# Kernel tuning notes

Hardware: AMD Instinct MI355X
Metric: run time of the kernel (lower is better)

Reference implementation:

```python
import jax, jax.numpy as jnp
import numpy as np

DIM = 128
N = 1024


def setup_inputs() -> dict:
    key = jax.random.key(0)
    ks = jax.random.split(key, 11)
    s = 1.0 / np.sqrt(DIM)
    # Linear params stored as [in, out] (y = x @ W + b), matching torch math.
    return {
        "x": jax.random.normal(ks[0], (N, DIM), jnp.float32),
        "W_Q": jax.random.uniform(ks[1], (DIM, DIM), jnp.float32, -s, s),
        "b_Q": jax.random.uniform(ks[2], (DIM,), jnp.float32, -s, s),
        "W_K": jax.random.uniform(ks[3], (DIM, DIM), jnp.float32, -s, s),
        "b_K": jax.random.uniform(ks[4], (DIM,), jnp.float32, -s, s),
        "W_V": jax.random.uniform(ks[5], (DIM, DIM), jnp.float32, -s, s),
        "b_V": jax.random.uniform(ks[6], (DIM,), jnp.float32, -s, s),
        "W_Ev": jax.random.uniform(ks[7], (DIM, DIM), jnp.float32, -s, s),
        "b_Ev": jax.random.uniform(ks[8], (DIM,), jnp.float32, -s, s),
        "W_A": jax.random.uniform(ks[9], (DIM, 1), jnp.float32, -s, s),
        "b_A": jax.random.uniform(ks[10], (1,), jnp.float32, -s, s),
    }


def reference(x, W_Q, b_Q, W_K, b_K, W_V, b_V, W_Ev, b_Ev, W_A, b_A):
    Q = x @ W_Q + b_Q                               # [n, d]
    K = x @ W_K + b_K                               # [n, d]
    V = x @ W_V + b_V                               # [n, d]
    edge_feat = jax.nn.relu(Q[:, None, :] + K[None, :, :])   # [n, n, d]
    e_ij = jnp.squeeze(edge_feat @ W_A, -1) + b_A[0]          # [n, n]
    alpha = jax.nn.softmax(e_ij, axis=1)                      # softmax over j
    EV = edge_feat @ W_Ev + b_Ev                              # [n, n, d]
    # out_i = sum_j alpha_ij * (V_j + EV_ij)
    out = jnp.einsum('ij,ijd->id', alpha, V[None, :, :] + EV)
    return out
```

## Files before the change

### kernel.cpp

```cpp
#include <hip/hip_runtime.h>

#define N 1024
#define DIM 128
#define TI 4
#define JCH 256
#define NCH 4
#define SC 16
#define NSC 16

template <int CTRL>
__device__ __forceinline__ float dpp_add(float x) {
  int y = __builtin_amdgcn_update_dpp(0, __float_as_int(x), CTRL, 0xF, 0xF, true);
  return x + __int_as_float(y);
}
__device__ __forceinline__ float red32(float x) {
  x = dpp_add<0x111>(x);
  x = dpp_add<0x112>(x);
  x = dpp_add<0x114>(x);
  x = dpp_add<0x118>(x);
  x = dpp_add<0x142>(x);
  return x;
}

__device__ __forceinline__ float bperm(int baddr, float x) {
  return __int_as_float(__builtin_amdgcn_ds_bpermute(baddr, __float_as_int(x)));
}

__device__ __forceinline__ float epart_keep(const float4 q, const float4 k,
                                            const float4 w, float4* relu) {
  const float rx = fmaxf(q.x + k.x, 0.f);
  const float ry = fmaxf(q.y + k.y, 0.f);
  const float rz = fmaxf(q.z + k.z, 0.f);
  const float rw = fmaxf(q.w + k.w, 0.f);
  relu->x = rx; relu->y = ry; relu->z = rz; relu->w = rw;
  float a = rx * w.x;
  a = fmaf(ry, w.y, a);
  a = fmaf(rz, w.z, a);
  a = fmaf(rw, w.w, a);
  return a;
}

__device__ __forceinline__ void accum_rs(float p, const float4 relu,
                                         const float4 v, float4* R, float4* S) {
  R->x = fmaf(p, relu.x, R->x);
  R->y = fmaf(p, relu.y, R->y);
  R->z = fmaf(p, relu.z, R->z);
  R->w = fmaf(p, relu.w, R->w);
  S->x = fmaf(p, v.x, S->x);
  S->y = fmaf(p, v.y, S->y);
  S->z = fmaf(p, v.z, S->z);
  S->w = fmaf(p, v.w, S->w);
}

__global__ __launch_bounds__(512) void qkv_kernel3(
    const float* __restrict__ x,
    const float* __restrict__ WQ, const float* __restrict__ bQ,
    const float* __restrict__ WK, const float* __restrict__ bK,
    const float* __restrict__ WV, const float* __restrict__ bV,
    float* __restrict__ Q, float* __restrict__ K, float* __restrict__ V) {
  const int i0 = blockIdx.x * 4;
  const int t = threadIdx.x;
  const int dq = t & 31;
  const int qr = t >> 5;

  __shared__ __align__(16) float xs[4][DIM];
  __shared__ __align__(16) float pacc[16][3][4][DIM];

  if (t < 128) {
    const int row = t >> 5, c4 = t & 31;
    ((float4*)&xs[row][0])[c4] = ((const float4*)(x + (i0 + row) * DIM))[c4];
  }
  __syncthreads();

  const float4* WQ4 = (const float4*)WQ;
  const float4* WK4 = (const float4*)WK;
  const float4* WV4 = (const float4*)WV;
  float4 aQ[4], aK[4], aV[4];
#pragma unroll
  for (int r = 0; r < 4; ++r) {
    aQ[r] = make_float4(0.f, 0.f, 0.f, 0.f);
    aK[r] = make_float4(0.f, 0.f, 0.f, 0.f);
    aV[r] = make_float4(0.f, 0.f, 0.f, 0.f);
  }
  const int c0 = qr * 8;
#pragma unroll 2
  for (int cc = 0; cc < 8; ++cc) {
    const int c = c0 + cc;
    const float4 wq = WQ4[c * 32 + dq];
    const float4 wk = WK4[c * 32 + dq];
    const float4 wv = WV4[c * 32 + dq];
#pragma unroll
    for (int r = 0; r < 4; ++r) {
      const float xv = xs[r][c];
      aQ[r].x = fmaf(xv, wq.x, aQ[r].x); aQ[r].y = fmaf(xv, wq.y, aQ[r].y);
      aQ[r].z = fmaf(xv, wq.z, aQ[r].z); aQ[r].w = fmaf(xv, wq.w, aQ[r].w);
      aK[r].x = fmaf(xv, wk.x, aK[r].x); aK[r].y = fmaf(xv, wk.y, aK[r].y);
      aK[r].z = fmaf(xv, wk.z, aK[r].z); aK[r].w = fmaf(xv, wk.w, aK[r].w);
      aV[r].x = fmaf(xv, wv.x, aV[r].x); aV[r].y = fmaf(xv, wv.y, aV[r].y);
      aV[r].z = fmaf(xv, wv.z, aV[r].z); aV[r].w = fmaf(xv, wv.w, aV[r].w);
    }
  }
#pragma unroll
  for (int r = 0; r < 4; ++r) {
    ((float4*)&pacc[qr][0][r][0])[dq] = aQ[r];
    ((float4*)&pacc[qr][1][r][0])[dq] = aK[r];
    ((float4*)&pacc[qr][2][r][0])[dq] = aV[r];
  }
  __syncthreads();
  {
    const int row = (t >> 7) & 3, d = t & 127;
#pragma unroll
    for (int m = 0; m < 3; ++m) {
      float s = 0.f;
#pragma unroll
      for (int c = 0; c < 16; ++c) s += pacc[c][m][row][d];
      float* dst = (m == 0) ? Q : (m == 1) ? K : V;
      const float* bias = (m == 0) ? bQ : (m == 1) ? bK : bV;
      dst[(i0 + row) * DIM + d] = s + bias[d];
    }
  }
}

__global__ __launch_bounds__(256, 4) void attn_fused6(
    const float* __restrict__ Q, const float* __restrict__ K,
    const float* __restrict__ V, const float* __restrict__ WA,
    float* __restrict__ Rw, float* __restrict__ Sw, float* __restrict__ Lw) {
  const int bi = blockIdx.x >> 2;
  const int jc = blockIdx.x & 3;
  const int i0 = bi * TI;
  const int j0 = jc * JCH;
  const int t = threadIdx.x;
  const int dq = t & 31;
  const int f = t >> 5;
  const int baddr = (t & 32) ? (63 << 2) : (31 << 2);

  __shared__ __align__(16) float red_s[2][8 * TI * DIM];
  __shared__ __align__(16) float4 lred4[8];

  float4 wa4 = ((const float4*)WA)[dq];
  const float LOG2E = 1.44269504088896340736f;
  wa4.x *= LOG2E; wa4.y *= LOG2E; wa4.z *= LOG2E; wa4.w *= LOG2E;

  float4 q4[TI];
#pragma unroll
  for (int r = 0; r < TI; ++r)
    q4[r] = ((const float4*)(Q + (i0 + r) * DIM))[dq];

  float4 Racc[TI], Sacc[TI];
#pragma unroll
  for (int r = 0; r < TI; ++r) {
    Racc[r] = make_float4(0.f, 0.f, 0.f, 0.f);
    Sacc[r] = make_float4(0.f, 0.f, 0.f, 0.f);
  }
  float4 lacc = make_float4(0.f, 0.f, 0.f, 0.f);

  const float4* K4 = (const float4*)K;
  const float4* V4 = (const float4*)V;
  float4 kc0 = K4[(j0 + f) * 32 + dq];
  float4 kc1 = K4[(j0 + 8 + f) * 32 + dq];
  float4 vc0 = V4[(j0 + f) * 32 + dq];
  float4 vc1 = V4[(j0 + 8 + f) * 32 + dq];

  for (int sc = 0; sc < NSC; ++sc) {
    const int jb = j0 + ((sc + 1 < NSC) ? sc + 1 : sc) * SC;

    float4 reluA0, reluA1, reluA2, reluA3;
    float4 peA;
    peA.x = epart_keep(q4[0], kc0, wa4, &reluA0);
    peA.y = epart_keep(q4[1], kc0, wa4, &reluA1);
    peA.z = epart_keep(q4[2], kc0, wa4, &reluA2);
    peA.w = epart_keep(q4[3], kc0, wa4, &reluA3);
    kc0 = K4[(jb + f) * 32 + dq];

    peA.x = red32(peA.x); peA.y = red32(peA.y);
    peA.z = red32(peA.z); peA.w = red32(peA.w);
    float4 pA;
    pA.x = __builtin_amdgcn_exp2f(bperm(baddr, peA.x));
    pA.y = __builtin_amdgcn_exp2f(bperm(baddr, peA.y));
    pA.z = __builtin_amdgcn_exp2f(bperm(baddr, peA.z));
    pA.w = __builtin_amdgcn_exp2f(bperm(baddr, peA.w));

    accum_rs(pA.x, reluA0, vc0, &Racc[0], &Sacc[0]);
    accum_rs(pA.y, reluA1, vc0, &Racc[1], &Sacc[1]);
    accum_rs(pA.z, reluA2, vc0, &Racc[2], &Sacc[2]);
    accum_rs(pA.w, reluA3, vc0, &Racc[3], &Sacc[3]);
    vc0 = V4[(jb + f) * 32 + dq];
    lacc.x += pA.x; lacc.y += pA.y; lacc.z += pA.z; lacc.w += pA.w;

    float4 reluB0, reluB1, reluB2, reluB3;
    float4 peB;
    peB.x = epart_keep(q4[0], kc1, wa4, &reluB0);
    peB.y = epart_keep(q4[1], kc1, wa4, &reluB1);
    peB.z = epart_keep(q4[2], kc1, wa4, &reluB2);
    peB.w = epart_keep(q4[3], kc1, wa4, &reluB3);
    kc1 = K4[(jb + 8 + f) * 32 + dq];

    peB.x = red32(peB.x); peB.y = red32(peB.y);
    peB.z = red32(peB.z); peB.w = red32(peB.w);
    float4 pB;
    pB.x = __builtin_amdgcn_exp2f(bperm(baddr, peB.x));
    pB.y = __builtin_amdgcn_exp2f(bperm(baddr, peB.y));
    pB.z = __builtin_amdgcn_exp2f(bperm(baddr, peB.z));
    pB.w = __builtin_amdgcn_exp2f(bperm(baddr, peB.w));

    accum_rs(pB.x, reluB0, vc1, &Racc[0], &Sacc[0]);
    accum_rs(pB.y, reluB1, vc1, &Racc[1], &Sacc[1]);
    accum_rs(pB.z, reluB2, vc1, &Racc[2], &Sacc[2]);
    accum_rs(pB.w, reluB3, vc1, &Racc[3], &Sacc[3]);
    vc1 = V4[(jb + 8 + f) * 32 + dq];
    lacc.x += pB.x; lacc.y += pB.y; lacc.z += pB.z; lacc.w += pB.w;
  }

  float4* F4r = (float4*)&red_s[0][0];
  float4* F4s = (float4*)&red_s[1][0];
#pragma unroll
  for (int r = 0; r < TI; ++r) {
    F4r[(f * 4 + r) * 32 + dq] = Racc[r];
    F4s[(f * 4 + r) * 32 + dq] = Sacc[r];
  }
  if (dq == 0) lred4[f] = lacc;
  __syncthreads();
#pragma unroll
  for (int p = 0; p < 4; ++p) {
    const int o = t + 256 * p;
    const int m = o >> 9;
    const int r = (o >> 7) & 3;
    const int d = o & 127;
    float acc = 0.f;
#pragma unroll
    for (int c = 0; c < 8; ++c) acc += red_s[m][(c * 4 + r) * 128 + d];
    float* dst = m ? Sw : Rw;
    dst[(jc * N + i0 + r) * DIM + d] = acc;
  }
  if (t < TI) {
    float l = 0.f;
#pragma unroll
    for (int c = 0; c < 8; ++c) l += ((const float*)&lred4[c])[t];
    Lw[jc * N + i0 + t] = l;
  }
}

__global__ __launch_bounds__(256) void attn_combine5(
    const float* __restrict__ WEv, const float* __restrict__ bEv,
    const float* __restrict__ Rw, const float* __restrict__ Sw,
    const float* __restrict__ Lw, float* __restrict__ out) {
  const int i0 = blockIdx.x * 2;
  const int t = threadIdx.x;

  __shared__ __align__(16) float Rst[2][DIM];
  __shared__ __align__(16) float Sst[2][DIM];
  __shared__ __align__(16) float4 Eacc4[8][2][DIM / 4];
  __shared__ float linv_s[2];

  if (t < 8) {
    const int row = t >> 2, c = t & 3;
    float l = Lw[c * N + i0 + row];
    l += __shfl_xor(l, 1, 4);
    l += __shfl_xor(l, 2, 4);
    if (c == 0) linv_s[row] = 1.0f / l;
  }

#pragma unroll
  for (int p = 0; p < 2; ++p) {
    const int o = t + 256 * p;
    const int d = o & 127;
    const int set = o >> 7;
    const int row = set & 1;
    const int mat = set >> 1;
    const float* src = mat ? Sw : Rw;
    float acc = 0.f;
#pragma unroll
    for (int c = 0; c < NCH; ++c) acc += src[(c * N + i0 + row) * DIM + d];
    if (mat) Sst[row][d] = acc; else Rst[row][d] = acc;
  }
  __syncthreads();

  {
    const int dq = t & 31;
    const int qr = t >> 5;
    const float4* WEv4 = (const float4*)WEv;
    float4 a0 = make_float4(0.f, 0.f, 0.f, 0.f);
    float4 a1 = make_float4(0.f, 0.f, 0.f, 0.f);
    const int dp0 = 16 * qr;
#pragma unroll 8
    for (int dp = dp0; dp < dp0 + 16; ++dp) {
      const float4 w4 = WEv4[dp * 32 + dq];
      const float r0 = Rst[0][dp];
      const float r1 = Rst[1][dp];
      a0.x = fmaf(r0, w4.x, a0.x); a0.y = fmaf(r0, w4.y, a0.y);
      a0.z = fmaf(r0, w4.z, a0.z); a0.w = fmaf(r0, w4.w, a0.w);
      a1.x = fmaf(r1, w4.x, a1.x); a1.y = fmaf(r1, w4.y, a1.y);
      a1.z = fmaf(r1, w4.z, a1.z); a1.w = fmaf(r1, w4.w, a1.w);
    }
    Eacc4[qr][0][dq] = a0;
    Eacc4[qr][1][dq] = a1;
  }
  __syncthreads();

  {
    const int row = t >> 7, d = t & 127;
    const int dq = d >> 2, e = d & 3;
    float acc = Sst[row][d];
#pragma unroll
    for (int qr = 0; qr < 8; ++qr)
      acc += ((const float*)&Eacc4[qr][row][dq])[e];
    out[(i0 + row) * DIM + d] = fmaf(acc, linv_s[row], bEv[d]);
  }
}

__global__ __launch_bounds__(256) void attn_fallback(
    const float* __restrict__ Q, const float* __restrict__ K,
    const float* __restrict__ V, const float* __restrict__ WA,
    const float* __restrict__ WEv, const float* __restrict__ bEv,
    float* __restrict__ out) {
  const int i = blockIdx.x;
  const int t = threadIdx.x;

  __shared__ __align__(16) float qs[DIM];
  __shared__ __align__(16) float was[DIM];
  __shared__ __align__(16) float p[N];
  __shared__ float red[256];
  __shared__ __align__(16) float Rs[8][DIM];
  __shared__ __align__(16) float Ss[8][DIM];

  if (t < DIM) {
    qs[t] = Q[i * DIM + t];
    was[t] = WA[t];
  }
  __syncthreads();

  float evals[4];
  float mloc = -3.4e38f;
  for (int jj = 0; jj < 4; ++jj) {
    const int j = t + jj * 256;
    const float4* krow = (const float4*)(K + j * DIM);
    const float4* q4p = (const float4*)qs;
    const float4* w4p = (const float4*)was;
    float acc = 0.f;
    for (int d4 = 0; d4 < DIM / 4; ++d4) {
      const float4 k4 = krow[d4];
      const float4 q4 = q4p[d4];
      const float4 w4 = w4p[d4];
      acc = fmaf(fmaxf(q4.x + k4.x, 0.f), w4.x, acc);
      acc = fmaf(fmaxf(q4.y + k4.y, 0.f), w4.y, acc);
      acc = fmaf(fmaxf(q4.z + k4.z, 0.f), w4.z, acc);
      acc = fmaf(fmaxf(q4.w + k4.w, 0.f), w4.w, acc);
    }
    evals[jj] = acc;
    mloc = fmaxf(mloc, acc);
  }
  red[t] = mloc;
  __syncthreads();
  for (int s = 128; s > 0; s >>= 1) {
    if (t < s) red[t] = fmaxf(red[t], red[t + s]);
    __syncthreads();
  }
  const float m = red[0];
  __syncthreads();
  float lsum = 0.f;
  for (int jj = 0; jj < 4; ++jj) {
    const float pe = __expf(evals[jj] - m);
    p[t + jj * 256] = pe;
    lsum += pe;
  }
  red[t] = lsum;
  __syncthreads();
  for (int s = 128; s > 0; s >>= 1) {
    if (t < s) red[t] += red[t + s];
    __syncthreads();
  }
  const float linv = 1.0f / red[0];
  __syncthreads();

  const int tx = t & 31;
  const int ty = t >> 5;
  const float4 q4 = ((const float4*)qs)[tx];
  float4 R4 = make_float4(0.f, 0.f, 0.f, 0.f);
  float4 S4 = make_float4(0.f, 0.f, 0.f, 0.f);
  for (int j = ty; j < N; j += 8) {
    const float pj = p[j];
    const float4 k4 = ((const float4*)(K + j * DIM))[tx];
    const float4 v4 = ((const float4*)(V + j * DIM))[tx];
    R4.x = fmaf(pj, fmaxf(q4.x + k4.x, 0.f), R4.x);
    R4.y = fmaf(pj, fmaxf(q4.y + k4.y, 0.f), R4.y);
    R4.z = fmaf(pj, fmaxf(q4.z + k4.z, 0.f), R4.z);
    R4.w = fmaf(pj, fmaxf(q4.w + k4.w, 0.f), R4.w);
    S4.x = fmaf(pj, v4.x, S4.x);
    S4.y = fmaf(pj, v4.y, S4.y);
    S4.z = fmaf(pj, v4.z, S4.z);
    S4.w = fmaf(pj, v4.w, S4.w);
  }
  ((float4*)&Rs[ty][0])[tx] = R4;
  ((float4*)&Ss[ty][0])[tx] = S4;
  __syncthreads();

  if (t < DIM) {
    float R = 0.f, S = 0.f;
    for (int g = 0; g < 8; ++g) {
      R += Rs[g][t];
      S += Ss[g][t];
    }
    Rs[0][t] = R;
    Ss[0][t] = S;
  }
  __syncthreads();

  if (t < DIM) {
    float o = Ss[0][t];
    for (int dp = 0; dp < DIM; ++dp) {
      o = fmaf(Rs[0][dp], WEv[dp * DIM + t], o);
    }
    out[i * DIM + t] = fmaf(o, linv, bEv[t]);
  }
}

extern "C" void kernel_launch(void* const* d_in, const int* in_sizes, int n_in,
                              void* d_out, int out_size, void* d_ws, size_t ws_size,
                              hipStream_t stream) {
  const float* x    = (const float*)d_in[0];
  const float* W_Q  = (const float*)d_in[1];
  const float* b_Q  = (const float*)d_in[2];
  const float* W_K  = (const float*)d_in[3];
  const float* b_K  = (const float*)d_in[4];
  const float* W_V  = (const float*)d_in[5];
  const float* b_V  = (const float*)d_in[6];
  const float* W_Ev = (const float*)d_in[7];
  const float* b_Ev = (const float*)d_in[8];
  const float* W_A  = (const float*)d_in[9];

  float* Q = (float*)d_ws;
  float* K = Q + N * DIM;
  float* V = K + N * DIM;
  float* out = (float*)d_out;

  const size_t need_floats = (size_t)3 * N * DIM + (size_t)2 * NCH * N * DIM +
                             (size_t)NCH * N;

  qkv_kernel3<<<N / 4, 512, 0, stream>>>(x, W_Q, b_Q, W_K, b_K, W_V, b_V, Q, K, V);

  if (ws_size >= need_floats * sizeof(float)) {
    float* Rw = V + N * DIM;
    float* Sw = Rw + NCH * N * DIM;
    float* Lw = Sw + NCH * N * DIM;
    attn_fused6<<<(N / TI) * NCH, 256, 0, stream>>>(Q, K, V, W_A, Rw, Sw, Lw);
    attn_combine5<<<N / 2, 256, 0, stream>>>(W_Ev, b_Ev, Rw, Sw, Lw, out);
  } else {
    attn_fallback<<<N, 256, 0, stream>>>(Q, K, V, W_A, W_Ev, b_Ev, out);
  }
}
```

Before: 111.0 us.

## Fuse attention split-j and combine kernels into one 1024-thread block per row tile

Replaces the two-kernel scheme (4 j-chunk blocks per 4-row tile writing partial R/S/L to workspace, then a combine kernel) with a single kernel. Each 1024-thread block covers all 1024 j for 4 rows and reduces partials across 32 wavefront groups in shared memory. It then applies W_Ev and the normalization in place. This removes the workspace round trip and one launch, but it cuts the grid from 1024 to 256 blocks and uses much larger shared memory (about 128KB of reduction buffers), which may lower occupancy and parallelism.

```diff
diff --git a/kernel.cpp b/kernel.cpp
--- a/kernel.cpp
+++ b/kernel.cpp
@@ -3,9 +3,7 @@
 #define N 1024
 #define DIM 128
 #define TI 4
-#define JCH 256
-#define NCH 4
-#define SC 16
+#define NG 32
 #define NSC 16
 
 template <int CTRL>
@@ -121,21 +119,22 @@
   }
 }
 
-__global__ __launch_bounds__(256, 4) void attn_fused6(
+__global__ __launch_bounds__(1024) void attn_mono(
     const float* __restrict__ Q, const float* __restrict__ K,
     const float* __restrict__ V, const float* __restrict__ WA,
-    float* __restrict__ Rw, float* __restrict__ Sw, float* __restrict__ Lw) {
-  const int bi = blockIdx.x >> 2;
-  const int jc = blockIdx.x & 3;
-  const int i0 = bi * TI;
-  const int j0 = jc * JCH;
+    const float* __restrict__ WEv, const float* __restrict__ bEv,
+    float* __restrict__ out) {
+  const int i0 = blockIdx.x * TI;
   const int t = threadIdx.x;
   const int dq = t & 31;
   const int f = t >> 5;
   const int baddr = (t & 32) ? (63 << 2) : (31 << 2);
 
-  __shared__ __align__(16) float red_s[2][8 * TI * DIM];
-  __shared__ __align__(16) float4 lred4[8];
+  __shared__ __align__(16) float red_s[2][NG * TI * DIM];
+  __shared__ __align__(16) float4 lred4[NG];
+  __shared__ __align__(16) float Rst[TI][DIM];
+  __shared__ __align__(16) float Sst[TI][DIM];
+  __shared__ float linv_s[TI];
 
   float4 wa4 = ((const float4*)WA)[dq];
   const float LOG2E = 1.44269504088896340736f;
@@ -156,13 +155,13 @@
 
   const float4* K4 = (const float4*)K;
   const float4* V4 = (const float4*)V;
-  float4 kc0 = K4[(j0 + f) * 32 + dq];
-  float4 kc1 = K4[(j0 + 8 + f) * 32 + dq];
-  float4 vc0 = V4[(j0 + f) * 32 + dq];
-  float4 vc1 = V4[(j0 + 8 + f) * 32 + dq];
+  float4 kc0 = K4[(f) * 32 + dq];
+  float4 kc1 = K4[(NG + f) * 32 + dq];
+  float4 vc0 = V4[(f) * 32 + dq];
+  float4 vc1 = V4[(NG + f) * 32 + dq];
 
   for (int sc = 0; sc < NSC; ++sc) {
-    const int jb = j0 + ((sc + 1 < NSC) ? sc + 1 : sc) * SC;
+    const int jb = ((sc + 1 < NSC) ? sc + 1 : sc) * (2 * NG);
 
     float4 reluA0, reluA1, reluA2, reluA3;
     float4 peA;
@@ -193,7 +192,7 @@
     peB.y = epart_keep(q4[1], kc1, wa4, &reluB1);
     peB.z = epart_keep(q4[2], kc1, wa4, &reluB2);
     peB.w = epart_keep(q4[3], kc1, wa4, &reluB3);
-    kc1 = K4[(jb + 8 + f) * 32 + dq];
+    kc1 = K4[(jb + NG + f) * 32 + dq];
 
     peB.x = red32(peB.x); peB.y = red32(peB.y);
     peB.z = red32(peB.z); peB.w = red32(peB.w);
@@ -207,7 +206,7 @@
     accum_rs(pB.y, reluB1, vc1, &Racc[1], &Sacc[1]);
     accum_rs(pB.z, reluB2, vc1, &Racc[2], &Sacc[2]);
     accum_rs(pB.w, reluB3, vc1, &Racc[3], &Sacc[3]);
-    vc1 = V4[(jb + 8 + f) * 32 + dq];
+    vc1 = V4[(jb + NG + f) * 32 + dq];
     lacc.x += pB.x; lacc.y += pB.y; lacc.z += pB.z; lacc.w += pB.w;
   }
 
@@ -220,91 +219,66 @@
   }
   if (dq == 0) lred4[f] = lacc;
   __syncthreads();
-#pragma unroll
-  for (int p = 0; p < 4; ++p) {
-    const int o = t + 256 * p;
-    const int m = o >> 9;
-    const int r = (o >> 7) & 3;
-    const int d = o & 127;
+
+  {
+    const int m = t >> 9;
+    const int r = (t >> 7) & 3;
+    const int d = t & 127;
     float acc = 0.f;
 #pragma unroll
-    for (int c = 0; c < 8; ++c) acc += red_s[m][(c * 4 + r) * 128 + d];
-    float* dst = m ? Sw : Rw;
-    dst[(jc * N + i0 + r) * DIM + d] = acc;
+    for (int c = 0; c < NG; ++c) acc += red_s[m][(c * 4 + r) * 128 + d];
+    if (m) Sst[r][d] = acc; else Rst[r][d] = acc;
   }
   if (t < TI) {
+    const float* lf = (const float*)lred4;
     float l = 0.f;
 #pragma unroll
-    for (int c = 0; c < 8; ++c) l += ((const float*)&lred4[c])[t];
-    Lw[jc * N + i0 + t] = l;
-  }
-}
-
-__global__ __launch_bounds__(256) void attn_combine5(
-    const float* __restrict__ WEv, const float* __restrict__ bEv,
-    const float* __restrict__ Rw, const float* __restrict__ Sw,
-    const float* __restrict__ Lw, float* __restrict__ out) {
-  const int i0 = blockIdx.x * 2;
-  const int t = threadIdx.x;
-
-  __shared__ __align__(16) float Rst[2][DIM];
-  __shared__ __align__(16) float Sst[2][DIM];
-  __shared__ __align__(16) float4 Eacc4[8][2][DIM / 4];
-  __shared__ float linv_s[2];
-
-  if (t < 8) {
-    const int row = t >> 2, c = t & 3;
-    float l = Lw[c * N + i0 + row];
-    l += __shfl_xor(l, 1, 4);
-    l += __shfl_xor(l, 2, 4);
-    if (c == 0) linv_s[row] = 1.0f / l;
-  }
-
-#pragma unroll
-  for (int p = 0; p < 2; ++p) {
-    const int o = t + 256 * p;
-    const int d = o & 127;
-    const int set = o >> 7;
-    const int row = set & 1;
-    const int mat = set >> 1;
-    const float* src = mat ? Sw : Rw;
-    float acc = 0.f;
-#pragma unroll
-    for (int c = 0; c < NCH; ++c) acc += src[(c * N + i0 + row) * DIM + d];
-    if (mat) Sst[row][d] = acc; else Rst[row][d] = acc;
+    for (int c = 0; c < NG; ++c) l += lf[c * 4 + t];
+    linv_s[t] = 1.0f / l;
   }
   __syncthreads();
 
   {
-    const int dq = t & 31;
-    const int qr = t >> 5;
+    const int qr = f;
     const float4* WEv4 = (const float4*)WEv;
     float4 a0 = make_float4(0.f, 0.f, 0.f, 0.f);
     float4 a1 = make_float4(0.f, 0.f, 0.f, 0.f);
-    const int dp0 = 16 * qr;
-#pragma unroll 8
-    for (int dp = dp0; dp < dp0 + 16; ++dp) {
+    float4 a2 = make_float4(0.f, 0.f, 0.f, 0.f);
+    float4 a3 = make_float4(0.f, 0.f, 0.f, 0.f);
+    const int dp0 = 4 * qr;
+#pragma unroll
+    for (int k = 0; k < 4; ++k) {
+      const int dp = dp0 + k;
       const float4 w4 = WEv4[dp * 32 + dq];
       const float r0 = Rst[0][dp];
       const float r1 = Rst[1][dp];
+      const float r2 = Rst[2][dp];
+      const float r3 = Rst[3][dp];
       a0.x = fmaf(r0, w4.x, a0.x); a0.y = fmaf(r0, w4.y, a0.y);
       a0.z = fmaf(r0, w4.z, a0.z); a0.w = fmaf(r0, w4.w, a0.w);
       a1.x = fmaf(r1, w4.x, a1.x); a1.y = fmaf(r1, w4.y, a1.y);
       a1.z = fmaf(r1, w4.z, a1.z); a1.w = fmaf(r1, w4.w, a1.w);
-    }
-    Eacc4[qr][0][dq] = a0;
-    Eacc4[qr][1][dq] = a1;
-  }
-  __syncthreads();
-
-  {
-    const int row = t >> 7, d = t & 127;
-    const int dq = d >> 2, e = d & 3;
-    float acc = Sst[row][d];
-#pragma unroll
-    for (int qr = 0; qr < 8; ++qr)
-      acc += ((const float*)&Eacc4[qr][row][dq])[e];
-    out[(i0 + row) * DIM + d] = fmaf(acc, linv_s[row], bEv[d]);
+      a2.x = fmaf(r2, w4.x, a2.x); a2.y = fmaf(r2, w4.y, a2.y);
+      a2.z = fmaf(r2, w4.z, a2.z); a2.w = fmaf(r2, w4.w, a2.w);
+      a3.x = fmaf(r3, w4.x, a3.x); a3.y = fmaf(r3, w4.y, a3.y);
+      a3.z = fmaf(r3, w4.z, a3.z); a3.w = fmaf(r3, w4.w, a3.w);
+    }
+    float4* Eq = (float4*)&red_s[0][0];
+    Eq[(qr * 4 + 0) * 32 + dq] = a0;
+    Eq[(qr * 4 + 1) * 32 + dq] = a1;
+    Eq[(qr * 4 + 2) * 32 + dq] = a2;
+    Eq[(qr * 4 + 3) * 32 + dq] = a3;
+  }
+  __syncthreads();
+
+  if (t < TI * DIM) {
+    const int r = t >> 7, d = t & 127;
+    float acc = Sst[r][d];
+    const float* Ef = &red_s[0][0];
+#pragma unroll
+    for (int qr = 0; qr < NG; ++qr)
+      acc += Ef[(qr * 4 + r) * 128 + d];
+    out[(i0 + r) * DIM + d] = fmaf(acc, linv_s[r], bEv[d]);
   }
 }
 
@@ -433,17 +407,12 @@
   float* V = K + N * DIM;
   float* out = (float*)d_out;
 
-  const size_t need_floats = (size_t)3 * N * DIM + (size_t)2 * NCH * N * DIM +
-                             (size_t)NCH * N;
+  const size_t need_floats = (size_t)3 * N * DIM;
 
   qkv_kernel3<<<N / 4, 512, 0, stream>>>(x, W_Q, b_Q, W_K, b_K, W_V, b_V, Q, K, V);
 
   if (ws_size >= need_floats * sizeof(float)) {
-    float* Rw = V + N * DIM;
-    float* Sw = Rw + NCH * N * DIM;
-    float* Lw = Sw + NCH * N * DIM;
-    attn_fused6<<<(N / TI) * NCH, 256, 0, stream>>>(Q, K, V, W_A, Rw, Sw, Lw);
-    attn_combine5<<<N / 2, 256, 0, stream>>>(W_Ev, b_Ev, Rw, Sw, Lw, out);
+    attn_mono<<<N / TI, 1024, 0, stream>>>(Q, K, V, W_A, W_Ev, b_Ev, out);
   } else {
     attn_fallback<<<N, 256, 0, stream>>>(Q, K, V, W_A, W_Ev, b_Ev, out);
   }
```

After: 105.1 us. 5.3% less time.
